# Kernel tuning notes

Hardware: AMD Instinct MI355X
Metric: run time of the kernel (lower is better)

The kernel has to match this reference:

```python
import jax, jax.numpy as jnp
import numpy as np

WS = 16          # window_size
N = WS * WS      # tokens per window
H = 8            # num_heads
HD = 64          # head_dim
DIM = 512
EPEG_K = 15
PAD = EPEG_K // 2


def _relative_position_index(ws):
    coords = np.stack(np.meshgrid(np.arange(ws), np.arange(ws), indexing='ij'))  # (2, ws, ws)
    flat = coords.reshape(2, -1)                                                 # (2, N)
    rel = flat[:, :, None] - flat[:, None, :]                                    # (2, N, N)
    rel = rel.transpose(1, 2, 0).astype(np.int64)                                # (N, N, 2)
    rel[..., 0] += ws - 1
    rel[..., 1] += ws - 1
    rel[..., 0] *= 2 * ws - 1
    return rel.sum(-1)                                                           # (N, N)

REL_IDX = jnp.asarray(_relative_position_index(WS), dtype=jnp.int32)


def setup_inputs() -> dict:
    key = jax.random.key(0)
    ks = jax.random.split(key, 8)
    B_ = 128
    x = jax.random.normal(ks[0], (B_, N, DIM), dtype=jnp.float32)
    qkv_w = jax.random.normal(ks[1], (3 * H * HD, DIM), dtype=jnp.float32) * 0.02
    qkv_b = jnp.zeros((3 * H * HD,), dtype=jnp.float32)
    pe_w = jax.random.normal(ks[2], (H, 1, EPEG_K, 1), dtype=jnp.float32) * 0.02  # depthwise (15,1) conv
    pe_b = jnp.zeros((H,), dtype=jnp.float32)
    rpb_table = jax.random.normal(ks[3], ((2 * WS - 1) * (2 * WS - 1), H), dtype=jnp.float32) * 0.02
    proj_w = jax.random.normal(ks[4], (DIM, H * HD), dtype=jnp.float32) * 0.02
    proj_b = jnp.zeros((DIM,), dtype=jnp.float32)
    return {"x": x, "qkv_w": qkv_w, "qkv_b": qkv_b, "pe_w": pe_w, "pe_b": pe_b,
            "rpb_table": rpb_table, "proj_w": proj_w, "proj_b": proj_b}


def reference(x, qkv_w, qkv_b, pe_w, pe_b, rpb_table, proj_w, proj_b):
    B_, n, _ = x.shape
    scale = HD ** -0.5
    qkv = (x @ qkv_w.T + qkv_b).reshape(B_, n, 3, H, HD).transpose(2, 0, 3, 1, 4)  # (3,B_,H,N,hd)
    q, k, v = qkv[0] * scale, qkv[1], qkv[2]
    attn = jnp.einsum('bhnd,bhmd->bhnm', q, k)                                    # (B_,H,N,N)
    # epeg: depthwise conv (k,1) over the score map, per head
    pe = jax.lax.conv_general_dilated(
        attn, pe_w, window_strides=(1, 1), padding=((PAD, PAD), (0, 0)),
        dimension_numbers=('NCHW', 'OIHW', 'NCHW'), feature_group_count=H)
    attn = attn + pe + pe_b[None, :, None, None]
    bias = rpb_table[REL_IDX.reshape(-1)].reshape(n, n, H).transpose(2, 0, 1)     # (H,N,N)
    attn = jax.nn.softmax(attn + bias[None], axis=-1)
    out = jnp.einsum('bhnm,bhmd->bnhd', attn, v).reshape(B_, n, H * HD)
    return out @ proj_w.T + proj_b
```

## Files before the change

kernel.cpp:

```cpp
#include <hip/hip_runtime.h>


typedef unsigned short u16;
typedef unsigned int u32;
typedef __attribute__((ext_vector_type(8))) short short8;
typedef __attribute__((ext_vector_type(4))) float f32x4;

__device__ __forceinline__ u16 f2bf(float f) {
  union { float f; u32 u; } v; v.f = f;
  return (u16)((v.u + 0x7FFFu + ((v.u >> 16) & 1u)) >> 16);
}
__device__ __forceinline__ float bf2f(u16 s) {
  union { u32 u; float f; } v; v.u = ((u32)s) << 16;
  return v.f;
}

__device__ __forceinline__ void gl2lds16(const u16* g, u16* l) {
  __builtin_amdgcn_global_load_lds((const __attribute__((address_space(1))) void*)g,
                                   (__attribute__((address_space(3))) void*)l, 16, 0, 0);
}

__device__ __forceinline__ int fragaddr(int frag, int lane) {
  return (frag * 64 + (lane ^ (frag & 7))) * 8;
}

__global__ __launch_bounds__(256) void cvt_all(
    const float* __restrict__ x, const float* __restrict__ w1f,
    const float* __restrict__ w2f, u16* __restrict__ xo,
    u16* __restrict__ w1o, u16* __restrict__ w2o) {
  const int NX = 4194304, NW1 = 196608, NW2 = 65536;
  int i = blockIdx.x * 256 + threadIdx.x;
  const float* src; u16* dst; int j;
  if (i < NX)                  { src = x;   dst = xo;  j = i; }
  else if (i < NX + NW1)       { src = w1f; dst = w1o; j = i - NX; }
  else if (i < NX + NW1 + NW2) { src = w2f; dst = w2o; j = i - NX - NW1; }
  else return;
  float4 f = ((const float4*)src)[j];
  uint2 o;
  o.x = (u32)f2bf(f.x) | ((u32)f2bf(f.y) << 16);
  o.y = (u32)f2bf(f.z) | ((u32)f2bf(f.w) << 16);
  ((uint2*)dst)[j] = o;
}

__device__ __forceinline__ void gemm256_core(
    const u16* __restrict__ A, const u16* __restrict__ B,
    int m0, int n0, u16* lds, f32x4 acc[8][4]) {
  const int NT = 8;
  int tid = threadIdx.x, wave = tid >> 6, lane = tid & 63;
  int wm = wave >> 2, wn = wave & 3;

  int ch0 = tid, ch1 = tid + 512;
  int row0 = ch0 >> 2, row1 = ch1 >> 2;
  int cg0 = (ch0 & 3) ^ (row0 & 3) ^ ((row0 >> 2) & 3);
  int cg1 = (ch1 & 3) ^ (row1 & 3) ^ ((row1 >> 2) & 3);
  const u16* Ag0 = A + (size_t)(m0 + row0) * 512 + cg0 * 8;
  const u16* Ag1 = A + (size_t)(m0 + row1) * 512 + cg1 * 8;
  const u16* Bg0 = B + (size_t)(n0 + row0) * 512 + cg0 * 8;
  const u16* Bg1 = B + (size_t)(n0 + row1) * 512 + cg1 * 8;
  int ldsu0 = wave * 64 * 8;
  int ldsu1 = (512 + wave * 64) * 8;

  int frag_off = (lane & 15) * 32 +
                 (((lane >> 4) ^ (lane & 3) ^ ((lane >> 2) & 3)) << 3);
  int abase = wm * 4096 + frag_off;
  int bbase = 8192 + wn * 2048 + frag_off;

#define STAGE(h)                                                             \
  do {                                                                       \
    if ((h) < NT * 4) {                                                      \
      int T_ = (h) >> 2, kh_ = ((h) >> 1) & 1, isB_ = (h) & 1;               \
      int ko_ = T_ * 64 + kh_ * 32;                                          \
      u16* d_ = lds + (T_ & 1) * 32768 + kh_ * 16384 + isB_ * 8192;          \
      gl2lds16((isB_ ? Bg0 : Ag0) + ko_, d_ + ldsu0);                        \
      gl2lds16((isB_ ? Bg1 : Ag1) + ko_, d_ + ldsu1);                        \
    }                                                                        \
  } while (0)

#define LDA(dst, mf, kh, p)                                                  \
  dst = *(const short8*)(lds + (p) * 32768 + (kh) * 16384 + abase + (mf) * 512)
#define LDB(dst, nf, kh, p)                                                  \
  dst = *(const short8*)(lds + (p) * 32768 + (kh) * 16384 + bbase + (nf) * 512)

#define MM16(M0)                                                                                   \
  __builtin_amdgcn_s_setprio(1);                                                                   \
  acc[(M0)+0][0] = __builtin_amdgcn_mfma_f32_16x16x32_bf16(a0, b0, acc[(M0)+0][0], 0, 0, 0);       \
  acc[(M0)+0][1] = __builtin_amdgcn_mfma_f32_16x16x32_bf16(a0, b1, acc[(M0)+0][1], 0, 0, 0);       \
  acc[(M0)+0][2] = __builtin_amdgcn_mfma_f32_16x16x32_bf16(a0, b2, acc[(M0)+0][2], 0, 0, 0);       \
  acc[(M0)+0][3] = __builtin_amdgcn_mfma_f32_16x16x32_bf16(a0, b3, acc[(M0)+0][3], 0, 0, 0);       \
  acc[(M0)+1][0] = __builtin_amdgcn_mfma_f32_16x16x32_bf16(a1, b0, acc[(M0)+1][0], 0, 0, 0);       \
  acc[(M0)+1][1] = __builtin_amdgcn_mfma_f32_16x16x32_bf16(a1, b1, acc[(M0)+1][1], 0, 0, 0);       \
  acc[(M0)+1][2] = __builtin_amdgcn_mfma_f32_16x16x32_bf16(a1, b2, acc[(M0)+1][2], 0, 0, 0);       \
  acc[(M0)+1][3] = __builtin_amdgcn_mfma_f32_16x16x32_bf16(a1, b3, acc[(M0)+1][3], 0, 0, 0);       \
  acc[(M0)+2][0] = __builtin_amdgcn_mfma_f32_16x16x32_bf16(a2, b0, acc[(M0)+2][0], 0, 0, 0);       \
  acc[(M0)+2][1] = __builtin_amdgcn_mfma_f32_16x16x32_bf16(a2, b1, acc[(M0)+2][1], 0, 0, 0);       \
  acc[(M0)+2][2] = __builtin_amdgcn_mfma_f32_16x16x32_bf16(a2, b2, acc[(M0)+2][2], 0, 0, 0);       \
  acc[(M0)+2][3] = __builtin_amdgcn_mfma_f32_16x16x32_bf16(a2, b3, acc[(M0)+2][3], 0, 0, 0);       \
  acc[(M0)+3][0] = __builtin_amdgcn_mfma_f32_16x16x32_bf16(a3, b0, acc[(M0)+3][0], 0, 0, 0);       \
  acc[(M0)+3][1] = __builtin_amdgcn_mfma_f32_16x16x32_bf16(a3, b1, acc[(M0)+3][1], 0, 0, 0);       \
  acc[(M0)+3][2] = __builtin_amdgcn_mfma_f32_16x16x32_bf16(a3, b2, acc[(M0)+3][2], 0, 0, 0);       \
  acc[(M0)+3][3] = __builtin_amdgcn_mfma_f32_16x16x32_bf16(a3, b3, acc[(M0)+3][3], 0, 0, 0);       \
  __builtin_amdgcn_s_setprio(0)

  STAGE(0); STAGE(1); STAGE(2); STAGE(3); STAGE(4);
  asm volatile("s_waitcnt vmcnt(6)" ::: "memory");
  __builtin_amdgcn_s_barrier();

#pragma unroll 1
  for (int kt = 0; kt < NT; ++kt) {
    int p = kt & 1;
    int hb = kt * 4 + 5;
    short8 a0, a1, a2, a3, b0, b1, b2, b3;
    LDA(a0, 0, 0, p); LDA(a1, 1, 0, p); LDA(a2, 2, 0, p); LDA(a3, 3, 0, p);
    LDB(b0, 0, 0, p); LDB(b1, 1, 0, p); LDB(b2, 2, 0, p); LDB(b3, 3, 0, p);
    STAGE(hb);
    __builtin_amdgcn_s_barrier();
    asm volatile("s_waitcnt lgkmcnt(0)" ::: "memory");
    MM16(0);
    __builtin_amdgcn_s_barrier();
    LDA(a0, 4, 0, p); LDA(a1, 5, 0, p); LDA(a2, 6, 0, p); LDA(a3, 7, 0, p);
    STAGE(hb + 1);
    __builtin_amdgcn_s_barrier();
    asm volatile("s_waitcnt lgkmcnt(0)" ::: "memory");
    MM16(4);
    if (kt == NT - 1) asm volatile("s_waitcnt vmcnt(0)" ::: "memory");
    else              asm volatile("s_waitcnt vmcnt(6)" ::: "memory");
    __builtin_amdgcn_s_barrier();
    LDA(a0, 0, 1, p); LDA(a1, 1, 1, p); LDA(a2, 2, 1, p); LDA(a3, 3, 1, p);
    LDB(b0, 0, 1, p); LDB(b1, 1, 1, p); LDB(b2, 2, 1, p); LDB(b3, 3, 1, p);
    STAGE(hb + 2);
    __builtin_amdgcn_s_barrier();
    asm volatile("s_waitcnt lgkmcnt(0)" ::: "memory");
    MM16(0);
    __builtin_amdgcn_s_barrier();
    LDA(a0, 4, 1, p); LDA(a1, 5, 1, p); LDA(a2, 6, 1, p); LDA(a3, 7, 1, p);
    STAGE(hb + 3);
    __builtin_amdgcn_s_barrier();
    asm volatile("s_waitcnt lgkmcnt(0)" ::: "memory");
    MM16(4);
    if (kt == NT - 2)     asm volatile("s_waitcnt vmcnt(4)" ::: "memory");
    else if (kt < NT - 2) asm volatile("s_waitcnt vmcnt(6)" ::: "memory");
    __builtin_amdgcn_s_barrier();
  }
#undef STAGE
#undef LDA
#undef LDB
#undef MM16
}

__global__ __launch_bounds__(512, 2) void gemm_qkv256(
    const u16* __restrict__ A, const u16* __restrict__ B,
    const float* __restrict__ qkvb, u16* __restrict__ qb,
    u16* __restrict__ kb, u16* __restrict__ vb) {
  __shared__ __align__(16) u16 lds[65536];
  f32x4 acc[8][4];
#pragma unroll
  for (int a = 0; a < 8; ++a)
#pragma unroll
    for (int c = 0; c < 4; ++c) acc[a][c] = (f32x4){0.f, 0.f, 0.f, 0.f};
  int bid = blockIdx.x;
  int wg = (bid & 7) * 96 + (bid >> 3);
  int m0 = (wg / 6) * 256, n0 = (wg % 6) * 256;
  gemm256_core(A, B, m0, n0, lds, acc);

  int tid = threadIdx.x, wave = tid >> 6, lane = tid & 63;
  int wm = wave >> 2, wn = wave & 3;
  int cx = lane & 15, g = lane >> 4;

  __syncthreads();
#pragma unroll
  for (int nf = 0; nf < 4; ++nf) {
    int cb = wn * 64 + nf * 16;
    int cgl = n0 + cb + cx;
    float bv = qkvb[cgl];
    float sc = ((cgl >> 9) == 0) ? 0.125f : 1.f;
#pragma unroll
    for (int mf = 0; mf < 8; ++mf) {
#pragma unroll
      for (int i = 0; i < 4; ++i) {
        int r = wm * 128 + mf * 16 + g * 4 + i;
        int c = cb + cx;
        int c16 = (c >> 3) ^ (((r >> 2) & 3) << 1);
        lds[r * 256 + c16 * 8 + (c & 7)] = f2bf((acc[mf][nf][i] + bv) * sc);
      }
    }
  }
  __syncthreads();

  int b = m0 >> 8;
#pragma unroll
  for (int j = 0; j < 16; ++j) {
    const int hg = j >> 2;
    int gcol = n0 + hg * 64;
    int which = gcol >> 9;
    int h = (gcol >> 6) & 7;
    u16* dst = (which == 0 ? qb : (which == 1 ? kb : vb)) +
               (size_t)(b * 8 + h) * 16384;
    int n = (j & 3) * 64 + (tid >> 3);
    int dc = tid & 7;
    int c16 = (hg * 8 + dc) ^ (((n >> 2) & 3) << 1);
    uint4 val = *(const uint4*)(lds + n * 256 + c16 * 8);
    *(uint4*)(dst + n * 64 + dc * 8) = val;
  }
}

__global__ __launch_bounds__(512, 2) void gemm_proj256(
    const u16* __restrict__ A, const u16* __restrict__ B,
    const float* __restrict__ pb, float* __restrict__ out) {
  __shared__ __align__(16) u16 lds[65536];
  f32x4 acc[8][4];
#pragma unroll
  for (int a = 0; a < 8; ++a)
#pragma unroll
    for (int c = 0; c < 4; ++c) acc[a][c] = (f32x4){0.f, 0.f, 0.f, 0.f};
  int bid = blockIdx.x;
  int wg = (bid & 7) * 32 + (bid >> 3);
  int m0 = (wg >> 1) * 256, n0 = (wg & 1) * 256;
  gemm256_core(A, B, m0, n0, lds, acc);
  int tid = threadIdx.x, wave = tid >> 6, lane = tid & 63;
  int wm = wave >> 2, wn = wave & 3;
  float bv[4];
#pragma unroll
  for (int nf = 0; nf < 4; ++nf)
    bv[nf] = pb[n0 + wn * 64 + nf * 16 + (lane & 15)];
#pragma unroll
  for (int mf = 0; mf < 8; ++mf) {
#pragma unroll
    for (int i = 0; i < 4; ++i) {
      int r = m0 + wm * 128 + mf * 16 + (lane >> 4) * 4 + i;
#pragma unroll
      for (int nf = 0; nf < 4; ++nf) {
        int c = n0 + wn * 64 + nf * 16 + (lane & 15);
        out[(size_t)r * 512 + c] = acc[mf][nf][i] + bv[nf];
      }
    }
  }
}

__global__ __launch_bounds__(256) void qconv(u16* __restrict__ qb,
                                             const float* __restrict__ pe_w) {
  __shared__ __align__(16) u16 Ql[256 * 72];
  __shared__ float w[15];
  int bh = blockIdx.x, h = bh & 7, tid = threadIdx.x;
  const uint4* src = (const uint4*)(qb + (size_t)bh * 16384);
#pragma unroll
  for (int it = 0; it < 8; ++it) {
    int idx = tid + it * 256;
    int row = idx >> 3, c = (idx & 7) * 8;
    *(uint4*)(Ql + row * 72 + c) = src[idx];
  }
  if (tid < 15) w[tid] = pe_w[h * 15 + tid] + (tid == 7 ? 1.f : 0.f);
  __syncthreads();
  int dg = (tid & 15) * 4, nb4 = tid >> 4;
  uint2* dst = (uint2*)(qb + (size_t)bh * 16384);
#pragma unroll
  for (int i = 0; i < 16; ++i) {
    int n = nb4 + i * 16;
    float a0 = 0.f, a1 = 0.f, a2 = 0.f, a3 = 0.f;
#pragma unroll
    for (int t = 0; t < 15; ++t) {
      int nn = n + t - 7;
      if (nn < 0 || nn > 255) continue;
      uint2 rv = *(const uint2*)(Ql + nn * 72 + dg);
      float wt = w[t];
      a0 += wt * bf2f(rv.x & 0xffff); a1 += wt * bf2f(rv.x >> 16);
      a2 += wt * bf2f(rv.y & 0xffff); a3 += wt * bf2f(rv.y >> 16);
    }
    uint2 pv;
    pv.x = (u32)f2bf(a0) | ((u32)f2bf(a1) << 16);
    pv.y = (u32)f2bf(a2) | ((u32)f2bf(a3) << 16);
    dst[(n * 64 + dg) >> 2] = pv;
  }
}

__global__ __launch_bounds__(512, 2) void attn_win(
    const u16* __restrict__ qb, const u16* __restrict__ kb,
    const u16* __restrict__ vb, const float* __restrict__ pe_b,
    const float* __restrict__ rpb, u16* __restrict__ attnout) {
  __shared__ __align__(16) u16 KfPs[21504];
  __shared__ __align__(16) u16 Vf[16384];
  __shared__ float biasl[961];
  __shared__ float pebs;

  int bh = blockIdx.x, b = bh >> 3, h = bh & 7;
  int tid = threadIdx.x, wave = tid >> 6, lane = tid & 63;
  int cx = lane & 15, g = lane >> 4;

  const uint4* kg = (const uint4*)(kb + (size_t)bh * 16384);
  const uint4* vg = (const uint4*)(vb + (size_t)bh * 16384);

  uint4 kreg[4];
#pragma unroll
  for (int it = 0; it < 4; ++it) kreg[it] = kg[tid + it * 512];

  u16* Vtmp = KfPs;
#pragma unroll
  for (int it = 0; it < 4; ++it) {
    int idx = tid + it * 512;
    uint4 v = vg[idx];
    int row = idx >> 3, c8 = (idx & 7) * 8;
    *(uint2*)(Vtmp + row * 68 + c8)     = make_uint2(v.x, v.y);
    *(uint2*)(Vtmp + row * 68 + c8 + 4) = make_uint2(v.z, v.w);
  }
  for (int i = tid; i < 961; i += 512) biasl[i] = rpb[i * 8 + h];
  if (tid == 0) pebs = pe_b[h];
  __syncthreads();

#pragma unroll
  for (int it = 0; it < 4; ++it) {
    int o = tid + it * 512;
    int frag = o >> 6, lanep = o & 63;
    int d = (frag >> 3) * 16 + (lanep & 15);
    int mb = (frag & 7) * 32 + (lanep >> 4) * 8;
    uint4 pk;
    pk.x = (u32)Vtmp[(mb + 0) * 68 + d] | ((u32)Vtmp[(mb + 1) * 68 + d] << 16);
    pk.y = (u32)Vtmp[(mb + 2) * 68 + d] | ((u32)Vtmp[(mb + 3) * 68 + d] << 16);
    pk.z = (u32)Vtmp[(mb + 4) * 68 + d] | ((u32)Vtmp[(mb + 5) * 68 + d] << 16);
    pk.w = (u32)Vtmp[(mb + 6) * 68 + d] | ((u32)Vtmp[(mb + 7) * 68 + d] << 16);
    *(uint4*)(Vf + (frag * 64 + (lanep ^ (frag & 7))) * 8) = pk;
  }
  __syncthreads();

  u16* Kf = KfPs;
#pragma unroll
  for (int it = 0; it < 4; ++it) {
    int idx = tid + it * 512;
    int n = idx >> 3, k8 = idx & 7;
    int frag = (n >> 4) * 2 + (k8 >> 2);
    int lanep = (n & 15) + 16 * (k8 & 3);
    *(uint4*)(Kf + (frag * 64 + (lanep ^ (frag & 7))) * 8) = kreg[it];
  }
  __syncthreads();

  u16* Psw = KfPs + 16384 + wave * 640;
  const u16* qgb = qb + (size_t)bh * 16384;

  for (int it2 = 0; it2 < 2; ++it2) {
    int qbase = it2 * 128 + wave * 16;
    const u16* qg = qgb + qbase * 64;
    short8 qf0 = *(const short8*)(qg + cx * 64 + g * 8);
    short8 qf1 = *(const short8*)(qg + cx * 64 + 32 + g * 8);

    float m_run[4] = {-1e30f, -1e30f, -1e30f, -1e30f};
    float l_run[4] = {0.f, 0.f, 0.f, 0.f};
    f32x4 oacc[4];
#pragma unroll
    for (int dt = 0; dt < 4; ++dt) oacc[dt] = (f32x4){0.f, 0.f, 0.f, 0.f};

#pragma unroll
    for (int c = 0; c < 2; ++c) {
      f32x4 acc[8];
#pragma unroll
      for (int mt = 0; mt < 8; ++mt) acc[mt] = (f32x4){0.f, 0.f, 0.f, 0.f};
#pragma unroll
      for (int mt = 0; mt < 8; ++mt) {
        int fr = (c * 8 + mt) * 2;
        short8 k0 = *(const short8*)(Kf + fragaddr(fr, lane));
        short8 k1 = *(const short8*)(Kf + fragaddr(fr + 1, lane));
        acc[mt] = __builtin_amdgcn_mfma_f32_16x16x32_bf16(qf0, k0, acc[mt], 0, 0, 0);
        acc[mt] = __builtin_amdgcn_mfma_f32_16x16x32_bf16(qf1, k1, acc[mt], 0, 0, 0);
      }

      float alpha4[4];
#pragma unroll
      for (int i = 0; i < 4; ++i) {
        int qtok = qbase + g * 4 + i;
        int bbase = ((qtok >> 4) - c * 8 + 15) * 31 + (qtok & 15) - cx + 15;
#pragma unroll
        for (int mt = 0; mt < 8; ++mt) acc[mt][i] += pebs + biasl[bbase - 31 * mt];
        float mx = acc[0][i];
#pragma unroll
        for (int mt = 1; mt < 8; ++mt) mx = fmaxf(mx, acc[mt][i]);
        mx = fmaxf(mx, __shfl_xor(mx, 1));
        mx = fmaxf(mx, __shfl_xor(mx, 2));
        mx = fmaxf(mx, __shfl_xor(mx, 4));
        mx = fmaxf(mx, __shfl_xor(mx, 8));
        float mnew = fmaxf(m_run[i], mx);
        float al = __expf(m_run[i] - mnew);
        float s = 0.f;
#pragma unroll
        for (int mt = 0; mt < 8; ++mt) {
          float e = __expf(acc[mt][i] - mnew);
          acc[mt][i] = e; s += e;
        }
        s += __shfl_xor(s, 1);
        s += __shfl_xor(s, 2);
        s += __shfl_xor(s, 4);
        s += __shfl_xor(s, 8);
        l_run[i] = l_run[i] * al + s;
        m_run[i] = mnew;
        alpha4[i] = al;
      }
#pragma unroll
      for (int dt = 0; dt < 4; ++dt)
#pragma unroll
        for (int i = 0; i < 4; ++i) oacc[dt][i] *= alpha4[i];

#pragma unroll
      for (int kk = 0; kk < 4; ++kk) {
#pragma unroll
        for (int t2 = 0; t2 < 2; ++t2)
#pragma unroll
          for (int i = 0; i < 4; ++i)
            Psw[(g * 4 + i) * 40 + t2 * 16 + cx] = f2bf(acc[kk * 2 + t2][i]);
        short8 pa = *(const short8*)(Psw + cx * 40 + g * 8);
#pragma unroll
        for (int dt = 0; dt < 4; ++dt) {
          short8 vf = *(const short8*)(Vf + fragaddr(dt * 8 + c * 4 + kk, lane));
          oacc[dt] = __builtin_amdgcn_mfma_f32_16x16x32_bf16(pa, vf, oacc[dt], 0, 0, 0);
        }
      }
    }

    float inv4[4];
#pragma unroll
    for (int i = 0; i < 4; ++i) inv4[i] = 1.f / l_run[i];
#pragma unroll
    for (int dt = 0; dt < 4; ++dt)
#pragma unroll
      for (int i = 0; i < 4; ++i)
        attnout[((size_t)b * 256 + qbase + g * 4 + i) * 512 + h * 64 + dt * 16 + cx]
            = f2bf(oacc[dt][i] * inv4[i]);
  }
}

extern "C" void kernel_launch(void* const* d_in, const int* in_sizes, int n_in,
                              void* d_out, int out_size, void* d_ws, size_t ws_size,
                              hipStream_t stream) {
  const float* x      = (const float*)d_in[0];
  const float* qkv_w  = (const float*)d_in[1];
  const float* qkv_b  = (const float*)d_in[2];
  const float* pe_w   = (const float*)d_in[3];
  const float* pe_b   = (const float*)d_in[4];
  const float* rpb    = (const float*)d_in[5];
  const float* proj_w = (const float*)d_in[6];
  const float* proj_b = (const float*)d_in[7];
  float* out = (float*)d_out;
  char* ws = (char*)d_ws;

  size_t off = 0;
  u16* xbf = (u16*)(ws + off); off += (size_t)16777216 * 2;
  u16* w1  = (u16*)(ws + off); off += (size_t)786432 * 2;
  u16* w2  = (u16*)(ws + off); off += (size_t)262144 * 2;
  u16* qb  = (u16*)(ws + off); off += (size_t)16777216 * 2;
  u16* kb  = (u16*)(ws + off); off += (size_t)16777216 * 2;
  u16* vb  = (u16*)(ws + off); off += (size_t)16777216 * 2;

  hipLaunchKernelGGL(cvt_all, dim3(17408), dim3(256), 0, stream,
                     x, qkv_w, proj_w, xbf, w1, w2);
  hipLaunchKernelGGL(gemm_qkv256, dim3(768), dim3(512), 0, stream,
                     xbf, w1, qkv_b, qb, kb, vb);
  hipLaunchKernelGGL(qconv, dim3(1024), dim3(256), 0, stream, qb, pe_w);
  hipLaunchKernelGGL(attn_win, dim3(1024), dim3(512), 0, stream,
                     qb, kb, vb, pe_b, rpb, xbf);
  hipLaunchKernelGGL(gemm_proj256, dim3(256), dim3(512), 0, stream,
                     xbf, w2, proj_b, out);
}
```

Before: 323.9 us.

## Transpose QK^T MFMA so each lane owns one query row in softmax

Swaps the MFMA operand order so the score tile is transposed and each lane holds one query's scores. The row max and sum then need two cross-lane shuffles instead of four per row, and each lane keeps one running max/sum. P is packed to bf16 with v_cvt_pk_bf16_f32 and written to LDS as 64-bit stores instead of scalar u16 stores. It also folds pe_b into the bias table, prefetches Q fragments before the staging phase, and sets wave priority around the MFMA blocks. In exchange it needs extra shuffles to broadcast the rescale factor and the inverse sum back to the output layout.

Result: faster. 294.0 us (-9.2%).

```diff
diff --git a/kernel.cpp b/kernel.cpp
--- a/kernel.cpp
+++ b/kernel.cpp
@@ -13,6 +13,11 @@
 __device__ __forceinline__ float bf2f(u16 s) {
   union { u32 u; float f; } v; v.u = ((u32)s) << 16;
   return v.f;
+}
+__device__ __forceinline__ u32 cvtpk(float lo, float hi) {
+  u32 r;
+  asm("v_cvt_pk_bf16_f32 %0, %1, %2" : "=v"(r) : "v"(lo), "v"(hi));
+  return r;
 }
 
 __device__ __forceinline__ void gl2lds16(const u16* g, u16* l) {
@@ -279,7 +284,6 @@
   __shared__ __align__(16) u16 KfPs[21504];
   __shared__ __align__(16) u16 Vf[16384];
   __shared__ float biasl[961];
-  __shared__ float pebs;
 
   int bh = blockIdx.x, b = bh >> 3, h = bh & 7;
   int tid = threadIdx.x, wave = tid >> 6, lane = tid & 63;
@@ -287,6 +291,12 @@
 
   const uint4* kg = (const uint4*)(kb + (size_t)bh * 16384);
   const uint4* vg = (const uint4*)(vb + (size_t)bh * 16384);
+  const u16* qgb = qb + (size_t)bh * 16384;
+
+  short8 qfr0a = *(const short8*)(qgb + (0 * 128 + wave * 16 + cx) * 64 + g * 8);
+  short8 qfr0b = *(const short8*)(qgb + (0 * 128 + wave * 16 + cx) * 64 + 32 + g * 8);
+  short8 qfr1a = *(const short8*)(qgb + (1 * 128 + wave * 16 + cx) * 64 + g * 8);
+  short8 qfr1b = *(const short8*)(qgb + (1 * 128 + wave * 16 + cx) * 64 + 32 + g * 8);
 
   uint4 kreg[4];
 #pragma unroll
@@ -301,8 +311,10 @@
     *(uint2*)(Vtmp + row * 68 + c8)     = make_uint2(v.x, v.y);
     *(uint2*)(Vtmp + row * 68 + c8 + 4) = make_uint2(v.z, v.w);
   }
-  for (int i = tid; i < 961; i += 512) biasl[i] = rpb[i * 8 + h];
-  if (tid == 0) pebs = pe_b[h];
+  {
+    float peb = pe_b[h];
+    for (int i = tid; i < 961; i += 512) biasl[i] = rpb[i * 8 + h] + peb;
+  }
   __syncthreads();
 
 #pragma unroll
@@ -332,16 +344,14 @@
   __syncthreads();
 
   u16* Psw = KfPs + 16384 + wave * 640;
-  const u16* qgb = qb + (size_t)bh * 16384;
-
+
+#pragma unroll
   for (int it2 = 0; it2 < 2; ++it2) {
+    short8 qf0 = it2 ? qfr1a : qfr0a;
+    short8 qf1 = it2 ? qfr1b : qfr0b;
     int qbase = it2 * 128 + wave * 16;
-    const u16* qg = qgb + qbase * 64;
-    short8 qf0 = *(const short8*)(qg + cx * 64 + g * 8);
-    short8 qf1 = *(const short8*)(qg + cx * 64 + 32 + g * 8);
-
-    float m_run[4] = {-1e30f, -1e30f, -1e30f, -1e30f};
-    float l_run[4] = {0.f, 0.f, 0.f, 0.f};
+
+    float m_run = -1e30f, l_run = 0.f;
     f32x4 oacc[4];
 #pragma unroll
     for (int dt = 0; dt < 4; ++dt) oacc[dt] = (f32x4){0.f, 0.f, 0.f, 0.f};
@@ -351,69 +361,78 @@
       f32x4 acc[8];
 #pragma unroll
       for (int mt = 0; mt < 8; ++mt) acc[mt] = (f32x4){0.f, 0.f, 0.f, 0.f};
+      __builtin_amdgcn_s_setprio(1);
 #pragma unroll
       for (int mt = 0; mt < 8; ++mt) {
         int fr = (c * 8 + mt) * 2;
         short8 k0 = *(const short8*)(Kf + fragaddr(fr, lane));
         short8 k1 = *(const short8*)(Kf + fragaddr(fr + 1, lane));
-        acc[mt] = __builtin_amdgcn_mfma_f32_16x16x32_bf16(qf0, k0, acc[mt], 0, 0, 0);
-        acc[mt] = __builtin_amdgcn_mfma_f32_16x16x32_bf16(qf1, k1, acc[mt], 0, 0, 0);
+        acc[mt] = __builtin_amdgcn_mfma_f32_16x16x32_bf16(k0, qf0, acc[mt], 0, 0, 0);
+        acc[mt] = __builtin_amdgcn_mfma_f32_16x16x32_bf16(k1, qf1, acc[mt], 0, 0, 0);
       }
-
-      float alpha4[4];
-#pragma unroll
-      for (int i = 0; i < 4; ++i) {
-        int qtok = qbase + g * 4 + i;
-        int bbase = ((qtok >> 4) - c * 8 + 15) * 31 + (qtok & 15) - cx + 15;
-#pragma unroll
-        for (int mt = 0; mt < 8; ++mt) acc[mt][i] += pebs + biasl[bbase - 31 * mt];
-        float mx = acc[0][i];
-#pragma unroll
-        for (int mt = 1; mt < 8; ++mt) mx = fmaxf(mx, acc[mt][i]);
-        mx = fmaxf(mx, __shfl_xor(mx, 1));
-        mx = fmaxf(mx, __shfl_xor(mx, 2));
-        mx = fmaxf(mx, __shfl_xor(mx, 4));
-        mx = fmaxf(mx, __shfl_xor(mx, 8));
-        float mnew = fmaxf(m_run[i], mx);
-        float al = __expf(m_run[i] - mnew);
-        float s = 0.f;
-#pragma unroll
-        for (int mt = 0; mt < 8; ++mt) {
+      __builtin_amdgcn_s_setprio(0);
+
+      int nb = (it2 * 8 + wave - c * 8 + 15) * 31 + cx - g * 4 + 15;
+#pragma unroll
+      for (int mt = 0; mt < 8; ++mt) {
+        const float* bp = biasl + (nb - 31 * mt);
+        acc[mt][0] += bp[0];  acc[mt][1] += bp[-1];
+        acc[mt][2] += bp[-2]; acc[mt][3] += bp[-3];
+      }
+
+      float mx = fmaxf(fmaxf(acc[0][0], acc[0][1]), fmaxf(acc[0][2], acc[0][3]));
+#pragma unroll
+      for (int mt = 1; mt < 8; ++mt)
+        mx = fmaxf(mx, fmaxf(fmaxf(acc[mt][0], acc[mt][1]),
+                             fmaxf(acc[mt][2], acc[mt][3])));
+      mx = fmaxf(mx, __shfl_xor(mx, 16));
+      mx = fmaxf(mx, __shfl_xor(mx, 32));
+      float mnew = fmaxf(m_run, mx);
+      float al = __expf(m_run - mnew);
+      float s = 0.f;
+#pragma unroll
+      for (int mt = 0; mt < 8; ++mt)
+#pragma unroll
+        for (int i = 0; i < 4; ++i) {
           float e = __expf(acc[mt][i] - mnew);
           acc[mt][i] = e; s += e;
         }
-        s += __shfl_xor(s, 1);
-        s += __shfl_xor(s, 2);
-        s += __shfl_xor(s, 4);
-        s += __shfl_xor(s, 8);
-        l_run[i] = l_run[i] * al + s;
-        m_run[i] = mnew;
-        alpha4[i] = al;
-      }
+      s += __shfl_xor(s, 16);
+      s += __shfl_xor(s, 32);
+      l_run = l_run * al + s;
+      m_run = mnew;
+
+      float alr[4];
+#pragma unroll
+      for (int i = 0; i < 4; ++i) alr[i] = __shfl(al, g * 4 + i);
 #pragma unroll
       for (int dt = 0; dt < 4; ++dt)
 #pragma unroll
-        for (int i = 0; i < 4; ++i) oacc[dt][i] *= alpha4[i];
+        for (int i = 0; i < 4; ++i) oacc[dt][i] *= alr[i];
 
 #pragma unroll
       for (int kk = 0; kk < 4; ++kk) {
-#pragma unroll
-        for (int t2 = 0; t2 < 2; ++t2)
-#pragma unroll
-          for (int i = 0; i < 4; ++i)
-            Psw[(g * 4 + i) * 40 + t2 * 16 + cx] = f2bf(acc[kk * 2 + t2][i]);
+        u32 w0 = cvtpk(acc[2 * kk][0], acc[2 * kk][1]);
+        u32 w1 = cvtpk(acc[2 * kk][2], acc[2 * kk][3]);
+        u32 w2 = cvtpk(acc[2 * kk + 1][0], acc[2 * kk + 1][1]);
+        u32 w3 = cvtpk(acc[2 * kk + 1][2], acc[2 * kk + 1][3]);
+        *(uint2*)(Psw + cx * 40 + g * 4)      = make_uint2(w0, w1);
+        *(uint2*)(Psw + cx * 40 + 16 + g * 4) = make_uint2(w2, w3);
         short8 pa = *(const short8*)(Psw + cx * 40 + g * 8);
+        __builtin_amdgcn_s_setprio(1);
 #pragma unroll
         for (int dt = 0; dt < 4; ++dt) {
           short8 vf = *(const short8*)(Vf + fragaddr(dt * 8 + c * 4 + kk, lane));
           oacc[dt] = __builtin_amdgcn_mfma_f32_16x16x32_bf16(pa, vf, oacc[dt], 0, 0, 0);
         }
+        __builtin_amdgcn_s_setprio(0);
       }
     }
 
+    float inv = 1.f / l_run;
     float inv4[4];
 #pragma unroll
-    for (int i = 0; i < 4; ++i) inv4[i] = 1.f / l_run[i];
+    for (int i = 0; i < 4; ++i) inv4[i] = __shfl(inv, g * 4 + i);
 #pragma unroll
     for (int dt = 0; dt < 4; ++dt)
 #pragma unroll
```
